# Kernel optimization log

Hardware: AMD Instinct MI355X
Metric: run time of the kernel (lower is better)

The kernel has to match this reference:

```python
import jax, jax.numpy as jnp
import numpy as np
from jax import lax

KERNEL = 5  # cv2 np.ones((5,5)) structuring element
EDGE_WEIGHT = 0.1


def _edge_weights(target):
    # target: [B,1,H,W] float. Binary mask -> morphological gradient via
    # max-pool (dilate) and min-pool (erode) with 5x5 window, SAME padding.
    # cv2 pads dilate with -inf and erode with +inf, so padding never
    # creates or removes foreground; reduce_window init values match that.
    b = (target > 0.5).astype(target.dtype)
    win = (1, 1, KERNEL, KERNEL)
    ones = (1, 1, 1, 1)
    dilated = lax.reduce_window(b, jnp.float32(-jnp.inf), lax.max, win, ones, 'SAME')
    eroded = lax.reduce_window(b, jnp.float32(jnp.inf), lax.min, win, ones, 'SAME')
    edge = dilated - eroded
    # Samples with empty masks get edge==0 everywhere, so the per-sample
    # binary_mask.sum()>0 guard in the original is a no-op here.
    return jnp.where(edge > 0, jnp.float32(EDGE_WEIGHT), jnp.float32(1.0))


def setup_inputs() -> dict:
    key = jax.random.key(0)
    k1, k2 = jax.random.split(key)
    shape = (32, 1, 1024, 1024)
    pred = jax.random.normal(k1, shape, dtype=jnp.float32)
    target = jax.random.randint(k2, shape, 0, 2).astype(jnp.float32)
    return {"pred": pred, "target": target}


def reference(pred, target):
    # BCEWithLogitsLoss(reduction='none'): softplus(x) - x*t (stable form)
    loss = jax.nn.softplus(pred) - pred * target
    # Weighting branch only taken when target.max()==1 and target.min()==0
    cond = jnp.logical_and(target.max() == 1.0, target.min() == 0.0)
    weights = _edge_weights(target)
    weights = jnp.where(cond, weights, jnp.float32(1.0))
    return (loss * weights).mean()
```

## Files before the change

### kernel.cpp

```cpp
#include <hip/hip_runtime.h>


#define IMG   1024
#define NTOT  33554432.0
#define NF4   8388608LL
#define GRID  2048

typedef unsigned long long u64;

__device__ __forceinline__ unsigned encf(float f) {
    unsigned u = __float_as_uint(f);
    return (u & 0x80000000u) ? ~u : (u | 0x80000000u);
}
__device__ __forceinline__ float decf(unsigned e) {
    unsigned u = (e & 0x80000000u) ? (e & 0x7fffffffu) : ~e;
    return __uint_as_float(u);
}

__global__ void bbl_init(double* dws, unsigned* uws) {
    if (threadIdx.x == 0) {
        dws[0] = 0.0; dws[1] = 0.0;
        uws[0] = 0xFFFFFFFFu;
        uws[1] = 0u;
    }
}

__global__ __launch_bounds__(256) void bbl_mask(
        const float* __restrict__ target, u64* __restrict__ Bm,
        unsigned* __restrict__ uws) {
    __shared__ unsigned rmn[4], rmx[4];
    const int tid = threadIdx.x, lane = tid & 63, wid = tid >> 6;
    const long long stride = (long long)GRID * 256;
    float vmin = 3.4e38f, vmax = -3.4e38f;

    for (long long q = (long long)blockIdx.x * 256 + tid; q < NF4; q += stride) {
        float4 v = ((const float4*)target)[q];
        vmin = fminf(vmin, fminf(fminf(v.x, v.y), fminf(v.z, v.w)));
        vmax = fmaxf(vmax, fmaxf(fmaxf(v.x, v.y), fmaxf(v.z, v.w)));
        u64 b0 = __ballot(v.x > 0.5f);
        u64 b1 = __ballot(v.y > 0.5f);
        u64 b2 = __ballot(v.z > 0.5f);
        u64 b3 = __ballot(v.w > 0.5f);
        if (lane < 4) {
            u64 val = (lane == 0) ? b0 : (lane == 1) ? b1 : (lane == 2) ? b2 : b3;
            long long q0 = q - lane;
            Bm[(q0 >> 4) + lane] = val;
        }
    }
    for (int off = 32; off > 0; off >>= 1) {
        vmin = fminf(vmin, __shfl_down(vmin, off));
        vmax = fmaxf(vmax, __shfl_down(vmax, off));
    }
    if (lane == 0) { rmn[wid] = encf(vmin); rmx[wid] = encf(vmax); }
    __syncthreads();
    if (tid == 0) {
        unsigned mn = rmn[0], mx = rmx[0];
        #pragma unroll
        for (int i = 1; i < 4; ++i) { mn = min(mn, rmn[i]); mx = max(mx, rmx[i]); }
        atomicMin(&uws[0], mn);
        atomicMax(&uws[1], mx);
    }
}

__global__ __launch_bounds__(256) void bbl_edge(
        const u64* __restrict__ Bm, u64* __restrict__ Em) {
    const int t  = blockIdx.x * 256 + threadIdx.x;
    const int w  = t & 15;
    const int rw = t >> 4;
    const int r  = rw & 1023;
    const u64* B = Bm + (((long long)(rw >> 10)) << 14);
    const int lo = max(r - 2, 0), hi = min(r + 2, IMG - 1);

    u64 vd[7], ve[7];
    #pragma unroll
    for (int j = 0; j < 7; ++j) {
        const int wj = w - 3 + j;
        if (wj < 0 || wj > 15) { vd[j] = 0ULL; ve[j] = ~0ULL; }
        else {
            u64 o = 0ULL, a = ~0ULL;
            for (int g = lo; g <= hi; ++g) { u64 b = B[g * 16 + wj]; o |= b; a &= b; }
            vd[j] = o; ve[j] = a;
        }
    }
    const int k = w & 3;
    u64 hd = vd[3], he = ve[3];
    #pragma unroll
    for (int di = 0; di < 4; ++di) {
        const int d = (di < 2) ? di - 2 : di - 1;
        const int kp = k + d;
        u64 td, te;
        if (kp >= 0 && kp <= 3) { td = vd[3 + d];                     te = ve[3 + d]; }
        else if (kp > 3)        { td = (vd[3 + d - 4] >> 1) | (vd[3 + d] << 63);
                                  te = (ve[3 + d - 4] >> 1) | (ve[3 + d] << 63); }
        else                    { td = (vd[3 + d + 4] << 1) | (vd[3 + d] >> 63);
                                  te = (ve[3 + d + 4] << 1) | (ve[3 + d] >> 63); }
        hd |= td; he &= te;
    }
    Em[t] = hd & ~he;
}

__global__ __launch_bounds__(256) void bbl_loss(
        const float* __restrict__ pred, const u64* __restrict__ Bm,
        const u64* __restrict__ Em, double* __restrict__ dws) {
    __shared__ float rs1[4], rse[4];
    const int tid = threadIdx.x, lane = tid & 63, wid = tid >> 6;
    const long long stride = (long long)GRID * 256;
    float s1 = 0.f, se = 0.f;

    for (long long q = (long long)blockIdx.x * 256 + tid; q < NF4; q += stride) {
        float4 p = ((const float4*)pred)[q];
        const long long wb = (q >> 6) << 2;
        const int l = (int)(q & 63);
        u64 t0 = Bm[wb + 0], t1 = Bm[wb + 1], t2 = Bm[wb + 2], t3 = Bm[wb + 3];
        u64 e0 = Em[wb + 0], e1 = Em[wb + 1], e2 = Em[wb + 2], e3 = Em[wb + 3];
        float x, loss;
        x = p.x;
        loss = fmaxf(x, 0.f) + __logf(1.f + __expf(-fabsf(x)))
             - (((t0 >> l) & 1ULL) ? x : 0.f);
        s1 += loss; se += ((e0 >> l) & 1ULL) ? loss : 0.f;
        x = p.y;
        loss = fmaxf(x, 0.f) + __logf(1.f + __expf(-fabsf(x)))
             - (((t1 >> l) & 1ULL) ? x : 0.f);
        s1 += loss; se += ((e1 >> l) & 1ULL) ? loss : 0.f;
        x = p.z;
        loss = fmaxf(x, 0.f) + __logf(1.f + __expf(-fabsf(x)))
             - (((t2 >> l) & 1ULL) ? x : 0.f);
        s1 += loss; se += ((e2 >> l) & 1ULL) ? loss : 0.f;
        x = p.w;
        loss = fmaxf(x, 0.f) + __logf(1.f + __expf(-fabsf(x)))
             - (((t3 >> l) & 1ULL) ? x : 0.f);
        s1 += loss; se += ((e3 >> l) & 1ULL) ? loss : 0.f;
    }

    for (int off = 32; off > 0; off >>= 1) {
        s1 += __shfl_down(s1, off);
        se += __shfl_down(se, off);
    }
    if (lane == 0) { rs1[wid] = s1; rse[wid] = se; }
    __syncthreads();
    if (tid == 0) {
        float S1 = rs1[0] + rs1[1] + rs1[2] + rs1[3];
        float Se = rse[0] + rse[1] + rse[2] + rse[3];
        atomicAdd(&dws[0], (double)S1);
        atomicAdd(&dws[1], (double)Se);
    }
}

__global__ void bbl_fin(const double* __restrict__ dws,
                        const unsigned* __restrict__ uws,
                        float* __restrict__ out) {
    if (threadIdx.x == 0) {
        float fmin = decf(uws[0]);
        float fmax = decf(uws[1]);
        bool cond = (fmax == 1.0f) && (fmin == 0.0f);
        double s = cond ? (dws[0] - 0.9 * dws[1]) : dws[0];
        out[0] = (float)(s / NTOT);
    }
}

__device__ __forceinline__ u64 shfl64(u64 v, int src) {
    unsigned lo = (unsigned)__shfl((int)(unsigned)(v & 0xffffffffULL), src, 64);
    unsigned hi = (unsigned)__shfl((int)(unsigned)(v >> 32), src, 64);
    return ((u64)hi << 32) | lo;
}
__device__ __forceinline__ u64 bcast64(u64 v, int srcImm) {
    unsigned lo = (unsigned)__builtin_amdgcn_readlane((int)(unsigned)(v & 0xffffffffULL), srcImm);
    unsigned hi = (unsigned)__builtin_amdgcn_readlane((int)(unsigned)(v >> 32), srcImm);
    return ((u64)hi << 32) | lo;
}

__global__ __launch_bounds__(256) void bbl_fallback(
        const float* __restrict__ pred,
        const float* __restrict__ target,
        double* __restrict__ dws, unsigned* __restrict__ uws) {
    __shared__ float    redS1[4], redSe[4];
    __shared__ unsigned redMn[4], redMx[4];
    const int tid = threadIdx.x, lane = tid & 63, wid = tid >> 6;
    const int gw = blockIdx.x * 4 + wid;
    const int img = gw >> 7;
    const int r0 = (gw & 127) * 8;
    const size_t base = (size_t)img * IMG * IMG;
    const float* tbase = target + base;
    const float* pbase = pred + base;
    const int w = lane & 15, k = w & 3;
    float vmin = 3.4e38f, vmax = -3.4e38f, s1 = 0.f, se = 0.f;

    auto loadrow = [&](int gr, bool mm) -> u64 {
        const float4* rp = (const float4*)(tbase + (size_t)gr * IMG);
        u64 myw = 0ULL;
        #pragma unroll
        for (int it = 0; it < 4; ++it) {
            float4 v = rp[it * 64 + lane];
            if (mm) {
                vmin = fminf(vmin, fminf(fminf(v.x, v.y), fminf(v.z, v.w)));
                vmax = fmaxf(vmax, fmaxf(fmaxf(v.x, v.y), fmaxf(v.z, v.w)));
            }
            u64 b0 = __ballot(v.x > 0.5f), b1 = __ballot(v.y > 0.5f);
            u64 b2 = __ballot(v.z > 0.5f), b3 = __ballot(v.w > 0.5f);
            u64 bw = (k == 0) ? b0 : (k == 1) ? b1 : (k == 2) ? b2 : b3;
            if ((w >> 2) == it) myw = bw;
        }
        return myw;
    };

    u64 q0 = loadrow(max(r0 - 2, 0), false);
    u64 q1 = loadrow(max(r0 - 1, 0), false);
    u64 q2 = loadrow(r0, true);
    u64 q3 = loadrow(r0 + 1, true);

    for (int r = r0; r < r0 + 8; ++r) {
        const int nr = min(r + 2, IMG - 1);
        u64 q4 = loadrow(nr, r + 2 <= r0 + 7);
        const float4* pp = (const float4*)(pbase + (size_t)r * IMG);
        float4 p0 = pp[0 * 64 + lane], p1 = pp[1 * 64 + lane];
        float4 p2 = pp[2 * 64 + lane], p3 = pp[3 * 64 + lane];
        u64 vd = q0 | q1 | q2 | q3 | q4;
        u64 ve = q0 & q1 & q2 & q3 & q4;
        u64 ct = q2, hd = vd, he = ve;
        #pragma unroll
        for (int di = 0; di < 4; ++di) {
            const int d = (di < 2) ? di - 2 : di - 1;
            int wp = w + d;
            bool inp = (wp >= 0) && (wp < 16);
            u64 ad = shfl64(vd, wp & 15), ae = shfl64(ve, wp & 15);
            ad = inp ? ad : 0ULL; ae = inp ? ae : ~0ULL;
            int ws2 = wp + ((d > 0) ? -4 : 4);
            u64 bd = shfl64(vd, ws2 & 15), be = shfl64(ve, ws2 & 15);
            int kp = k + d;
            u64 rd, re;
            if (d > 0) {
                rd = (kp <= 3) ? ad : ((bd >> 1) | (ad << 63));
                re = (kp <= 3) ? ae : ((be >> 1) | (ae << 63));
            } else {
                rd = (kp >= 0) ? ad : ((bd << 1) | (ad >> 63));
                re = (kp >= 0) ? ae : ((be << 1) | (ae >> 63));
            }
            hd |= rd; he &= re;
        }
        u64 em = hd & ~he;
        #pragma unroll
        for (int it = 0; it < 4; ++it) {
            float4 p = (it == 0) ? p0 : (it == 1) ? p1 : (it == 2) ? p2 : p3;
            #pragma unroll
            for (int m = 0; m < 4; ++m) {
                u64 ew = bcast64(em, it * 4 + m);
                u64 tw = bcast64(ct, it * 4 + m);
                float x = (m == 0) ? p.x : (m == 1) ? p.y : (m == 2) ? p.z : p.w;
                float xt = ((tw >> lane) & 1ULL) ? x : 0.f;
                float loss = fmaxf(x, 0.f) + __logf(1.f + __expf(-fabsf(x))) - xt;
                s1 += loss; se += ((ew >> lane) & 1ULL) ? loss : 0.f;
            }
        }
        q0 = q1; q1 = q2; q2 = q3; q3 = q4;
    }
    for (int off = 32; off > 0; off >>= 1) {
        s1 += __shfl_down(s1, off); se += __shfl_down(se, off);
        vmin = fminf(vmin, __shfl_down(vmin, off));
        vmax = fmaxf(vmax, __shfl_down(vmax, off));
    }
    if (lane == 0) {
        redS1[wid] = s1; redSe[wid] = se;
        redMn[wid] = encf(vmin); redMx[wid] = encf(vmax);
    }
    __syncthreads();
    if (tid == 0) {
        float S1 = 0.f, Se = 0.f; unsigned mn = 0xFFFFFFFFu, mx = 0u;
        #pragma unroll
        for (int i = 0; i < 4; ++i) {
            S1 += redS1[i]; Se += redSe[i];
            mn = min(mn, redMn[i]); mx = max(mx, redMx[i]);
        }
        atomicAdd(&dws[0], (double)S1); atomicAdd(&dws[1], (double)Se);
        atomicMin(&uws[0], mn); atomicMax(&uws[1], mx);
    }
}

extern "C" void kernel_launch(void* const* d_in, const int* in_sizes, int n_in,
                              void* d_out, int out_size, void* d_ws, size_t ws_size,
                              hipStream_t stream) {
    const float* pred   = (const float*)d_in[0];
    const float* target = (const float*)d_in[1];
    double*   dws = (double*)d_ws;
    unsigned* uws = (unsigned*)((char*)d_ws + 16);
    float*    out = (float*)d_out;

    const size_t MASKB = 4194304;
    const size_t need  = 4096 + 2 * MASKB;
    u64* Bm = (u64*)((char*)d_ws + 4096);
    u64* Em = (u64*)((char*)d_ws + 4096 + MASKB);

    hipLaunchKernelGGL(bbl_init, dim3(1), dim3(64), 0, stream, dws, uws);
    if (ws_size >= need) {
        hipLaunchKernelGGL(bbl_mask, dim3(GRID), dim3(256), 0, stream, target, Bm, uws);
        hipLaunchKernelGGL(bbl_edge, dim3(GRID), dim3(256), 0, stream, Bm, Em);
        hipLaunchKernelGGL(bbl_loss, dim3(GRID), dim3(256), 0, stream, pred, Bm, Em, dws);
    } else {
        hipLaunchKernelGGL(bbl_fallback, dim3(1024), dim3(256), 0, stream,
                           pred, target, dws, uws);
    }
    hipLaunchKernelGGL(bbl_fin, dim3(1), dim3(64), 0, stream, dws, uws, out);
}
```

Measured before the change: 352.1 us.

## Interleave target and edge bits per float4 and batch loads in mask and loss

The edge kernel now has each thread handle four mask words and reuse the loaded row window across them. It also re-packs the target and edge bitmasks into a 4-bit-per-float4 interleaved layout, so the loss kernel reads one 16-byte word per 16 float4s instead of eight scattered 64-bit words. The mask and loss kernels replace grid-stride loops with fixed 16-iteration unrolled blocks, loading 8 float4s at once for more memory-level parallelism. This needs extra workspace and relies on the input size matching GRID exactly.

Result: faster. 340.3 us (-3.4%).

```diff
diff --git a/kernel.cpp b/kernel.cpp
--- a/kernel.cpp
+++ b/kernel.cpp
@@ -3,7 +3,7 @@
 
 #define IMG   1024
 #define NTOT  33554432.0
-#define NF4   8388608LL
+#define NF4   8388608
 #define GRID  2048
 
 typedef unsigned long long u64;
@@ -15,6 +15,14 @@
 __device__ __forceinline__ float decf(unsigned e) {
     unsigned u = (e & 0x80000000u) ? (e & 0x7fffffffu) : ~e;
     return __uint_as_float(u);
+}
+__device__ __forceinline__ u64 spread4(u64 x) {
+    x &= 0xFFFFULL;
+    x = (x | (x << 24)) & 0x000000FF000000FFULL;
+    x = (x | (x << 12)) & 0x000F000F000F000FULL;
+    x = (x | (x <<  6)) & 0x0303030303030303ULL;
+    x = (x | (x <<  3)) & 0x1111111111111111ULL;
+    return x;
 }
 
 __global__ void bbl_init(double* dws, unsigned* uws) {
@@ -30,21 +38,29 @@
         unsigned* __restrict__ uws) {
     __shared__ unsigned rmn[4], rmx[4];
     const int tid = threadIdx.x, lane = tid & 63, wid = tid >> 6;
-    const long long stride = (long long)GRID * 256;
+    const int qb = blockIdx.x * 4096 + tid;
+    const float4* T = (const float4*)target;
     float vmin = 3.4e38f, vmax = -3.4e38f;
 
-    for (long long q = (long long)blockIdx.x * 256 + tid; q < NF4; q += stride) {
-        float4 v = ((const float4*)target)[q];
-        vmin = fminf(vmin, fminf(fminf(v.x, v.y), fminf(v.z, v.w)));
-        vmax = fmaxf(vmax, fmaxf(fmaxf(v.x, v.y), fmaxf(v.z, v.w)));
-        u64 b0 = __ballot(v.x > 0.5f);
-        u64 b1 = __ballot(v.y > 0.5f);
-        u64 b2 = __ballot(v.z > 0.5f);
-        u64 b3 = __ballot(v.w > 0.5f);
-        if (lane < 4) {
-            u64 val = (lane == 0) ? b0 : (lane == 1) ? b1 : (lane == 2) ? b2 : b3;
-            long long q0 = q - lane;
-            Bm[(q0 >> 4) + lane] = val;
+    #pragma unroll
+    for (int half = 0; half < 2; ++half) {
+        float4 v[8];
+        #pragma unroll
+        for (int j = 0; j < 8; ++j) v[j] = T[qb + (half * 8 + j) * 256];
+        #pragma unroll
+        for (int j = 0; j < 8; ++j) {
+            float4 t = v[j];
+            vmin = fminf(vmin, fminf(fminf(t.x, t.y), fminf(t.z, t.w)));
+            vmax = fmaxf(vmax, fmaxf(fmaxf(t.x, t.y), fmaxf(t.z, t.w)));
+            u64 b0 = __ballot(t.x > 0.5f);
+            u64 b1 = __ballot(t.y > 0.5f);
+            u64 b2 = __ballot(t.z > 0.5f);
+            u64 b3 = __ballot(t.w > 0.5f);
+            if (lane < 4) {
+                const int q0 = qb - lane + (half * 8 + j) * 256;
+                u64 val = (lane == 0) ? b0 : (lane == 1) ? b1 : (lane == 2) ? b2 : b3;
+                Bm[(q0 >> 4) + lane] = val;
+            }
         }
     }
     for (int off = 32; off > 0; off >>= 1) {
@@ -63,73 +79,103 @@
 }
 
 __global__ __launch_bounds__(256) void bbl_edge(
-        const u64* __restrict__ Bm, u64* __restrict__ Em) {
-    const int t  = blockIdx.x * 256 + threadIdx.x;
-    const int w  = t & 15;
-    const int rw = t >> 4;
-    const int r  = rw & 1023;
-    const u64* B = Bm + (((long long)(rw >> 10)) << 14);
+        const u64* __restrict__ Bm, ulonglong2* __restrict__ TE) {
+    const int t   = blockIdx.x * 256 + threadIdx.x;
+    const int itg = t & 3;
+    const int r   = (t >> 2) & 1023;
+    const int img = t >> 12;
+    const u64* B  = Bm + img * 16384;
     const int lo = max(r - 2, 0), hi = min(r + 2, IMG - 1);
-
-    u64 vd[7], ve[7];
-    #pragma unroll
-    for (int j = 0; j < 7; ++j) {
-        const int wj = w - 3 + j;
-        if (wj < 0 || wj > 15) { vd[j] = 0ULL; ve[j] = ~0ULL; }
-        else {
-            u64 o = 0ULL, a = ~0ULL;
-            for (int g = lo; g <= hi; ++g) { u64 b = B[g * 16 + wj]; o |= b; a &= b; }
-            vd[j] = o; ve[j] = a;
-        }
-    }
-    const int k = w & 3;
-    u64 hd = vd[3], he = ve[3];
-    #pragma unroll
-    for (int di = 0; di < 4; ++di) {
-        const int d = (di < 2) ? di - 2 : di - 1;
-        const int kp = k + d;
-        u64 td, te;
-        if (kp >= 0 && kp <= 3) { td = vd[3 + d];                     te = ve[3 + d]; }
-        else if (kp > 3)        { td = (vd[3 + d - 4] >> 1) | (vd[3 + d] << 63);
-                                  te = (ve[3 + d - 4] >> 1) | (ve[3 + d] << 63); }
-        else                    { td = (vd[3 + d + 4] << 1) | (vd[3 + d] >> 63);
-                                  te = (ve[3 + d + 4] << 1) | (ve[3 + d] >> 63); }
-        hd |= td; he &= te;
-    }
-    Em[t] = hd & ~he;
+    const int w0 = 4 * itg - 4;
+
+    u64 vd[12], ve[12];
+    #pragma unroll
+    for (int j = 0; j < 12; ++j) { vd[j] = 0ULL; ve[j] = ~0ULL; }
+    for (int g = lo; g <= hi; ++g) {
+        u64 row[12];
+        #pragma unroll
+        for (int j = 0; j < 12; ++j) {
+            const int wj = w0 + j;
+            row[j] = B[g * 16 + min(max(wj, 0), 15)];
+        }
+        #pragma unroll
+        for (int j = 0; j < 12; ++j) {
+            const int wj = w0 + j;
+            const bool ok = (wj >= 0) && (wj <= 15);
+            vd[j] |= ok ? row[j] : 0ULL;
+            ve[j] &= ok ? row[j] : ~0ULL;
+        }
+    }
+    u64 em[4], ct[4];
+    #pragma unroll
+    for (int k = 0; k < 4; ++k) {
+        u64 hd = vd[4 + k], he = ve[4 + k];
+        #pragma unroll
+        for (int di = 0; di < 4; ++di) {
+            const int d  = (di < 2) ? di - 2 : di - 1;
+            const int kp = k + d;
+            u64 td, te2;
+            if (kp >= 0 && kp <= 3) { td = vd[4 + k + d];            te2 = ve[4 + k + d]; }
+            else if (kp > 3) { td  = (vd[k + d] >> 1) | (vd[4 + k + d] << 63);
+                               te2 = (ve[k + d] >> 1) | (ve[4 + k + d] << 63); }
+            else             { td  = (vd[8 + k + d] << 1) | (vd[4 + k + d] >> 63);
+                               te2 = (ve[8 + k + d] << 1) | (ve[4 + k + d] >> 63); }
+            hd |= td; he &= te2;
+        }
+        em[k] = hd & ~he;
+        ct[k] = B[r * 16 + 4 * itg + k];
+    }
+    const int Lbase = img * 16384 + r * 16 + 4 * itg;
+    #pragma unroll
+    for (int j = 0; j < 4; ++j) {
+        u64 tL = spread4(ct[0] >> (16 * j)) | (spread4(ct[1] >> (16 * j)) << 1)
+               | (spread4(ct[2] >> (16 * j)) << 2) | (spread4(ct[3] >> (16 * j)) << 3);
+        u64 eL = spread4(em[0] >> (16 * j)) | (spread4(em[1] >> (16 * j)) << 1)
+               | (spread4(em[2] >> (16 * j)) << 2) | (spread4(em[3] >> (16 * j)) << 3);
+        ulonglong2 o; o.x = tL; o.y = eL;
+        TE[Lbase + j] = o;
+    }
 }
 
 __global__ __launch_bounds__(256) void bbl_loss(
-        const float* __restrict__ pred, const u64* __restrict__ Bm,
-        const u64* __restrict__ Em, double* __restrict__ dws) {
+        const float* __restrict__ pred, const ulonglong2* __restrict__ TE,
+        double* __restrict__ dws) {
     __shared__ float rs1[4], rse[4];
     const int tid = threadIdx.x, lane = tid & 63, wid = tid >> 6;
-    const long long stride = (long long)GRID * 256;
+    const int qb = blockIdx.x * 4096 + tid;
+    const float4* P = (const float4*)pred;
     float s1 = 0.f, se = 0.f;
 
-    for (long long q = (long long)blockIdx.x * 256 + tid; q < NF4; q += stride) {
-        float4 p = ((const float4*)pred)[q];
-        const long long wb = (q >> 6) << 2;
-        const int l = (int)(q & 63);
-        u64 t0 = Bm[wb + 0], t1 = Bm[wb + 1], t2 = Bm[wb + 2], t3 = Bm[wb + 3];
-        u64 e0 = Em[wb + 0], e1 = Em[wb + 1], e2 = Em[wb + 2], e3 = Em[wb + 3];
-        float x, loss;
-        x = p.x;
-        loss = fmaxf(x, 0.f) + __logf(1.f + __expf(-fabsf(x)))
-             - (((t0 >> l) & 1ULL) ? x : 0.f);
-        s1 += loss; se += ((e0 >> l) & 1ULL) ? loss : 0.f;
-        x = p.y;
-        loss = fmaxf(x, 0.f) + __logf(1.f + __expf(-fabsf(x)))
-             - (((t1 >> l) & 1ULL) ? x : 0.f);
-        s1 += loss; se += ((e1 >> l) & 1ULL) ? loss : 0.f;
-        x = p.z;
-        loss = fmaxf(x, 0.f) + __logf(1.f + __expf(-fabsf(x)))
-             - (((t2 >> l) & 1ULL) ? x : 0.f);
-        s1 += loss; se += ((e2 >> l) & 1ULL) ? loss : 0.f;
-        x = p.w;
-        loss = fmaxf(x, 0.f) + __logf(1.f + __expf(-fabsf(x)))
-             - (((t3 >> l) & 1ULL) ? x : 0.f);
-        s1 += loss; se += ((e3 >> l) & 1ULL) ? loss : 0.f;
+    #pragma unroll
+    for (int half = 0; half < 2; ++half) {
+        float4 p[8]; ulonglong2 te[8];
+        #pragma unroll
+        for (int j = 0; j < 8; ++j) {
+            const int q = qb + (half * 8 + j) * 256;
+            p[j]  = P[q];
+            te[j] = TE[q >> 4];
+        }
+        #pragma unroll
+        for (int j = 0; j < 8; ++j) {
+            const int q  = qb + (half * 8 + j) * 256;
+            const int sh = (q & 15) * 4;
+            const unsigned tn = (unsigned)(te[j].x >> sh) & 0xFu;
+            const unsigned en = (unsigned)(te[j].y >> sh) & 0xFu;
+            const float4 v = p[j];
+            float x, loss;
+            x = v.x;
+            loss = fmaxf(x, 0.f) + __logf(1.f + __expf(-fabsf(x))) - ((tn & 1u) ? x : 0.f);
+            s1 += loss; se += (en & 1u) ? loss : 0.f;
+            x = v.y;
+            loss = fmaxf(x, 0.f) + __logf(1.f + __expf(-fabsf(x))) - ((tn & 2u) ? x : 0.f);
+            s1 += loss; se += (en & 2u) ? loss : 0.f;
+            x = v.z;
+            loss = fmaxf(x, 0.f) + __logf(1.f + __expf(-fabsf(x))) - ((tn & 4u) ? x : 0.f);
+            s1 += loss; se += (en & 4u) ? loss : 0.f;
+            x = v.w;
+            loss = fmaxf(x, 0.f) + __logf(1.f + __expf(-fabsf(x))) - ((tn & 8u) ? x : 0.f);
+            s1 += loss; se += (en & 8u) ? loss : 0.f;
+        }
     }
 
     for (int off = 32; off > 0; off >>= 1) {
@@ -139,10 +185,8 @@
     if (lane == 0) { rs1[wid] = s1; rse[wid] = se; }
     __syncthreads();
     if (tid == 0) {
-        float S1 = rs1[0] + rs1[1] + rs1[2] + rs1[3];
-        float Se = rse[0] + rse[1] + rse[2] + rse[3];
-        atomicAdd(&dws[0], (double)S1);
-        atomicAdd(&dws[1], (double)Se);
+        atomicAdd(&dws[0], (double)(rs1[0] + rs1[1] + rs1[2] + rs1[3]));
+        atomicAdd(&dws[1], (double)(rse[0] + rse[1] + rse[2] + rse[3]));
     }
 }
 
@@ -285,15 +329,15 @@
     float*    out = (float*)d_out;
 
     const size_t MASKB = 4194304;
-    const size_t need  = 4096 + 2 * MASKB;
-    u64* Bm = (u64*)((char*)d_ws + 4096);
-    u64* Em = (u64*)((char*)d_ws + 4096 + MASKB);
+    const size_t need  = 4096 + MASKB + 2 * MASKB;
+    u64*        Bm = (u64*)((char*)d_ws + 4096);
+    ulonglong2* TE = (ulonglong2*)((char*)d_ws + 4096 + MASKB);
 
     hipLaunchKernelGGL(bbl_init, dim3(1), dim3(64), 0, stream, dws, uws);
     if (ws_size >= need) {
         hipLaunchKernelGGL(bbl_mask, dim3(GRID), dim3(256), 0, stream, target, Bm, uws);
-        hipLaunchKernelGGL(bbl_edge, dim3(GRID), dim3(256), 0, stream, Bm, Em);
-        hipLaunchKernelGGL(bbl_loss, dim3(GRID), dim3(256), 0, stream, pred, Bm, Em, dws);
+        hipLaunchKernelGGL(bbl_edge, dim3(512), dim3(256), 0, stream, Bm, TE);
+        hipLaunchKernelGGL(bbl_loss, dim3(GRID), dim3(256), 0, stream, pred, TE, dws);
     } else {
         hipLaunchKernelGGL(bbl_fallback, dim3(1024), dim3(256), 0, stream,
                            pred, target, dws, uws);
```
